# Optimization experiments

Measured on AMD Instinct MI355X. Metric: run time of the kernel, lower is better.

## Reference

```python
import jax, jax.numpy as jnp
import numpy as np

N_NODES = 100000
N_EDGES = 1600000
D_IN = 64
D_OUT = 64
EDGE_DIM = 1


def setup_inputs() -> dict:
    key = jax.random.key(0)
    ks = jax.random.split(key, 6)
    x = jax.random.normal(ks[0], (N_NODES, D_IN), dtype=jnp.float32)
    edge_index = jax.random.randint(ks[1], (2, N_EDGES), 0, N_NODES, dtype=jnp.int64)
    edge_attr = jax.random.uniform(ks[2], (N_EDGES, EDGE_DIM), dtype=jnp.float32)
    # xavier-uniform-ish weight
    limit = float(np.sqrt(6.0 / (D_IN + D_OUT)))
    weight = jax.random.uniform(ks[3], (D_IN, D_OUT), minval=-limit, maxval=limit, dtype=jnp.float32)
    lim2 = float(np.sqrt(1.0 / EDGE_DIM))
    ew_W = jax.random.uniform(ks[4], (EDGE_DIM, D_OUT), minval=-lim2, maxval=lim2, dtype=jnp.float32)
    ew_b = jnp.zeros((D_OUT,), dtype=jnp.float32)
    bias = jnp.zeros((D_OUT,), dtype=jnp.float32)
    return {"x": x, "edge_index": edge_index, "edge_attr": edge_attr,
            "weight": weight, "ew_W": ew_W, "ew_b": ew_b, "bias": bias}


def reference(x, edge_index, edge_attr, weight, ew_W, ew_b, bias):
    n_nodes = x.shape[0]
    src = edge_index[0]  # i: message source
    dst = edge_index[1]  # j: message destination
    x_t = x @ weight                                   # [N, D_OUT]
    edge_w = jax.nn.sigmoid(edge_attr @ ew_W + ew_b)   # [E, D_OUT]
    msg = x_t[src] * edge_w                            # [E, D_OUT] gather-multiply
    out = jax.ops.segment_sum(msg, dst, num_segments=n_nodes)  # scatter-add
    return out + bias
```

## Files before the change

kernel.cpp:

```cpp
#include <hip/hip_runtime.h>
#include <hip/hip_bf16.h>
#include <math.h>

#define D 64
#define SLOTS 32
#define SPILL_CAP 65536

typedef __hip_bfloat16 bf16;
typedef __attribute__((ext_vector_type(8))) short bf16x8;
typedef __attribute__((ext_vector_type(4))) float f32x4;

static __device__ __forceinline__ short f2bf(float f) {
    unsigned u = __float_as_uint(f);
    u = (u + 0x7FFFu + ((u >> 16) & 1u)) >> 16;
    return (short)u;
}
static __device__ __forceinline__ float bf2f(unsigned short h) {
    return __uint_as_float(((unsigned)h) << 16);
}
static __device__ __forceinline__ float fsig(float a, float nwd, float nbd) {
    float e = __expf(fmaf(a, nwd, nbd));
    return __builtin_amdgcn_rcpf(1.f + e);
}

__global__ __launch_bounds__(256) void gemm_hist_kernel(const float* __restrict__ x,
                                                        const float* __restrict__ W,
                                                        const int* __restrict__ ei,
                                                        const float* __restrict__ ea,
                                                        bf16* __restrict__ xt,
                                                        int* __restrict__ counts,
                                                        long long* __restrict__ rankv,
                                                        int n_nodes, int n_edges,
                                                        int hist_blocks) {
    __shared__ float Ws[64 * 64];

    if ((int)blockIdx.x < hist_blocks) {
        const int gid = blockIdx.x * blockDim.x + threadIdx.x;
        const int nth = hist_blocks * blockDim.x;
        for (int e = gid; e < n_edges; e += nth) {
            int dst = ei[n_edges + e];
            unsigned v = ((unsigned)min((int)(ea[e] * 32768.f), 32767) << 17) | (unsigned)ei[e];
            int r = atomicAdd(&counts[dst], 1);
            rankv[e] = ((long long)v << 32) | (unsigned)r;
        }
        return;
    }

    const int bid = blockIdx.x - hist_blocks;
    {
        const float4* src = reinterpret_cast<const float4*>(W);
        float4* dstp = reinterpret_cast<float4*>(Ws);
        for (int i = threadIdx.x; i < 1024; i += 256) dstp[i] = src[i];
    }
    __syncthreads();

    const int lane  = threadIdx.x & 63;
    const int wv    = threadIdx.x >> 6;
    const int m0    = bid * 64 + wv * 16;
    const int half  = lane >> 4;
    const int idx16 = lane & 15;
    const int k0    = half * 8;

    bf16x8 bfrag[4][2];
#pragma unroll
    for (int t = 0; t < 4; ++t) {
#pragma unroll
        for (int h = 0; h < 2; ++h) {
            bf16x8 f;
#pragma unroll
            for (int j = 0; j < 8; ++j)
                f[j] = f2bf(Ws[(h * 32 + k0 + j) * 64 + t * 16 + idx16]);
            bfrag[t][h] = f;
        }
    }

    const int am = m0 + idx16;
    const bool valid = (am < n_nodes);
    const float* arow = x + (size_t)(valid ? am : 0) * 64;

    f32x4 acc[4] = {{0.f, 0.f, 0.f, 0.f}, {0.f, 0.f, 0.f, 0.f},
                    {0.f, 0.f, 0.f, 0.f}, {0.f, 0.f, 0.f, 0.f}};

#pragma unroll
    for (int h = 0; h < 2; ++h) {
        bf16x8 afrag = {0, 0, 0, 0, 0, 0, 0, 0};
        if (valid) {
            float4 p0 = *reinterpret_cast<const float4*>(arow + h * 32 + k0);
            float4 p1 = *reinterpret_cast<const float4*>(arow + h * 32 + k0 + 4);
            afrag[0] = f2bf(p0.x); afrag[1] = f2bf(p0.y);
            afrag[2] = f2bf(p0.z); afrag[3] = f2bf(p0.w);
            afrag[4] = f2bf(p1.x); afrag[5] = f2bf(p1.y);
            afrag[6] = f2bf(p1.z); afrag[7] = f2bf(p1.w);
        }
#pragma unroll
        for (int t = 0; t < 4; ++t)
            acc[t] = __builtin_amdgcn_mfma_f32_16x16x32_bf16(afrag, bfrag[t][h],
                                                             acc[t], 0, 0, 0);
    }

    const int srow0 = m0 + half * 4;
#pragma unroll
    for (int r = 0; r < 4; ++r) {
        int row = srow0 + r;
        if (row < n_nodes) {
#pragma unroll
            for (int t = 0; t < 4; ++t)
                xt[(size_t)row * 64 + t * 16 + idx16] = __float2bfloat16(acc[t][r]);
        }
    }
}

__global__ __launch_bounds__(256) void fill_kernel(const int* __restrict__ ei,
                                                   const long long* __restrict__ rankv,
                                                   unsigned* __restrict__ csr,
                                                   long long* __restrict__ spill,
                                                   int* __restrict__ spillcnt,
                                                   int n_edges) {
    int e = blockIdx.x * blockDim.x + threadIdx.x;
    if (e >= n_edges) return;
    long long rv = rankv[e];
    int r = (int)(unsigned)rv;
    unsigned v = (unsigned)(rv >> 32);
    int dst = ei[n_edges + e];
    if (r < SLOTS) {
        __builtin_nontemporal_store(v, csr + (((unsigned)dst) << 5) + r);
    } else {
        int sp = atomicAdd(spillcnt, 1);
        if (sp < SPILL_CAP) spill[sp] = ((long long)v << 17) | (unsigned)dst;
    }
}

__global__ __launch_bounds__(256) void gather_kernel(const int* __restrict__ counts,
                                                     const unsigned* __restrict__ csr,
                                                     const bf16* __restrict__ xt,
                                                     const float* __restrict__ ewW,
                                                     const float* __restrict__ ewb,
                                                     const float* __restrict__ bias,
                                                     float* __restrict__ out,
                                                     int n_nodes) {
    const int lane  = threadIdx.x & 63;
    const int sub   = lane >> 4;
    const int l     = lane & 15;
    const int d0    = l * 4;
    const int wavei = (blockIdx.x * blockDim.x + threadIdx.x) >> 6;
    const int node  = wavei * 4 + sub;
    if (node >= n_nodes) return;

    const float4 wv4 = *reinterpret_cast<const float4*>(ewW + d0);
    const float4 bv4 = *reinterpret_cast<const float4*>(ewb + d0);
    const float nw0 = -wv4.x, nw1 = -wv4.y, nw2 = -wv4.z, nw3 = -wv4.w;
    const float nb0 = -bv4.x, nb1 = -bv4.y, nb2 = -bv4.z, nb3 = -bv4.w;
    const float s15 = 1.f / 32768.f;

    int deg = counts[node];
    if (deg > SLOTS) deg = SLOTS;
    const unsigned base = ((unsigned)node) << 5;

    float acc0 = 0.f, acc1 = 0.f, acc2 = 0.f, acc3 = 0.f;
    int k = 0;
    for (; k + 8 <= deg; k += 8) {
        unsigned q[8];
        ushort4 rv[8];
#pragma unroll
        for (int j = 0; j < 8; ++j)
            q[j] = __builtin_nontemporal_load(csr + base + k + j);
#pragma unroll
        for (int j = 0; j < 8; ++j) {
            unsigned off = ((q[j] & 0x1FFFFu) << 6) + d0;
            rv[j] = *reinterpret_cast<const ushort4*>(xt + off);
        }
#pragma unroll
        for (int j = 0; j < 8; ++j) {
            float a = (float)(q[j] >> 17) * s15;
            acc0 = fmaf(bf2f(rv[j].x), fsig(a, nw0, nb0), acc0);
            acc1 = fmaf(bf2f(rv[j].y), fsig(a, nw1, nb1), acc1);
            acc2 = fmaf(bf2f(rv[j].z), fsig(a, nw2, nb2), acc2);
            acc3 = fmaf(bf2f(rv[j].w), fsig(a, nw3, nb3), acc3);
        }
    }
    for (; k + 4 <= deg; k += 4) {
        unsigned q[4];
        ushort4 rv[4];
#pragma unroll
        for (int j = 0; j < 4; ++j)
            q[j] = __builtin_nontemporal_load(csr + base + k + j);
#pragma unroll
        for (int j = 0; j < 4; ++j) {
            unsigned off = ((q[j] & 0x1FFFFu) << 6) + d0;
            rv[j] = *reinterpret_cast<const ushort4*>(xt + off);
        }
#pragma unroll
        for (int j = 0; j < 4; ++j) {
            float a = (float)(q[j] >> 17) * s15;
            acc0 = fmaf(bf2f(rv[j].x), fsig(a, nw0, nb0), acc0);
            acc1 = fmaf(bf2f(rv[j].y), fsig(a, nw1, nb1), acc1);
            acc2 = fmaf(bf2f(rv[j].z), fsig(a, nw2, nb2), acc2);
            acc3 = fmaf(bf2f(rv[j].w), fsig(a, nw3, nb3), acc3);
        }
    }
    for (; k < deg; ++k) {
        unsigned q = __builtin_nontemporal_load(csr + base + k);
        unsigned off = ((q & 0x1FFFFu) << 6) + d0;
        ushort4 rv = *reinterpret_cast<const ushort4*>(xt + off);
        float a = (float)(q >> 17) * s15;
        acc0 = fmaf(bf2f(rv.x), fsig(a, nw0, nb0), acc0);
        acc1 = fmaf(bf2f(rv.y), fsig(a, nw1, nb1), acc1);
        acc2 = fmaf(bf2f(rv.z), fsig(a, nw2, nb2), acc2);
        acc3 = fmaf(bf2f(rv.w), fsig(a, nw3, nb3), acc3);
    }
    f32x4 o;
    o.x = acc0 + bias[d0 + 0];
    o.y = acc1 + bias[d0 + 1];
    o.z = acc2 + bias[d0 + 2];
    o.w = acc3 + bias[d0 + 3];
    __builtin_nontemporal_store(o, reinterpret_cast<f32x4*>(out + (size_t)node * 64 + d0));
}

__global__ __launch_bounds__(256) void spill_kernel(const long long* __restrict__ spill,
                                                    const int* __restrict__ spillcnt,
                                                    const bf16* __restrict__ xt,
                                                    const float* __restrict__ ewW,
                                                    const float* __restrict__ ewb,
                                                    float* __restrict__ out) {
    int n = *spillcnt;
    if (n > SPILL_CAP) n = SPILL_CAP;
    const int gid = blockIdx.x * blockDim.x + threadIdx.x;
    const int d0 = (gid & 15) * 4;
    const int estride = (gridDim.x * blockDim.x) >> 4;
    const float s15 = 1.f / 32768.f;
    for (int e = gid >> 4; e < n; e += estride) {
        long long s = spill[e];
        int dst = (int)(s & 0x1FFFF);
        unsigned v = (unsigned)(s >> 17);
        int src = (int)(v & 0x1FFFFu);
        float a = (float)(v >> 17) * s15;
        float* op = out + (size_t)dst * 64 + d0;
        const bf16* xp = xt + (size_t)src * 64 + d0;
#pragma unroll
        for (int j = 0; j < 4; ++j) {
            float w = fsig(a, -ewW[d0 + j], -ewb[d0 + j]);
            unsafeAtomicAdd(op + j, __bfloat162float(xp[j]) * w);
        }
    }
}

__global__ __launch_bounds__(256) void init_out_kernel(float* __restrict__ out,
                                                       const float* __restrict__ bias,
                                                       int n_f4) {
    int i = blockIdx.x * blockDim.x + threadIdx.x;
    if (i >= n_f4) return;
    float4 b4 = reinterpret_cast<const float4*>(bias)[i & 15];
    reinterpret_cast<float4*>(out)[i] = b4;
}

__global__ __launch_bounds__(256) void edge_atomic_kernel(const int* __restrict__ ei,
                                                          const float* __restrict__ ea,
                                                          const bf16* __restrict__ xt,
                                                          const float* __restrict__ ewW,
                                                          const float* __restrict__ ewb,
                                                          float* __restrict__ out,
                                                          int n_edges) {
    const int gid = blockIdx.x * blockDim.x + threadIdx.x;
    const int d0 = (gid & 15) * 4;
    int e = gid >> 4;
    const int estride = (gridDim.x * blockDim.x) >> 4;
    for (; e < n_edges; e += estride) {
        const int src = ei[e];
        const int dst = ei[n_edges + e];
        const float a = ea[e];
        float xv0 = __bfloat162float(xt[(size_t)src * 64 + d0 + 0]);
        float xv1 = __bfloat162float(xt[(size_t)src * 64 + d0 + 1]);
        float xv2 = __bfloat162float(xt[(size_t)src * 64 + d0 + 2]);
        float xv3 = __bfloat162float(xt[(size_t)src * 64 + d0 + 3]);
        float w0 = fsig(a, -ewW[d0 + 0], -ewb[d0 + 0]);
        float w1 = fsig(a, -ewW[d0 + 1], -ewb[d0 + 1]);
        float w2 = fsig(a, -ewW[d0 + 2], -ewb[d0 + 2]);
        float w3 = fsig(a, -ewW[d0 + 3], -ewb[d0 + 3]);
        float* op = out + (size_t)dst * 64 + d0;
        unsafeAtomicAdd(op + 0, xv0 * w0);
        unsafeAtomicAdd(op + 1, xv1 * w1);
        unsafeAtomicAdd(op + 2, xv2 * w2);
        unsafeAtomicAdd(op + 3, xv3 * w3);
    }
}

extern "C" void kernel_launch(void* const* d_in, const int* in_sizes, int n_in,
                              void* d_out, int out_size, void* d_ws, size_t ws_size,
                              hipStream_t stream) {
    const float* x      = (const float*)d_in[0];
    const int*   ei     = (const int*)d_in[1];
    const float* ea     = (const float*)d_in[2];
    const float* weight = (const float*)d_in[3];
    const float* ewW    = (const float*)d_in[4];
    const float* ewb    = (const float*)d_in[5];
    const float* bias   = (const float*)d_in[6];
    float* out = (float*)d_out;

    const int n_nodes = in_sizes[0] / D;
    const int n_edges = in_sizes[2];

    char* ws = (char*)d_ws;
    const size_t xt_bytes    = (size_t)n_nodes * D * sizeof(bf16);
    const size_t cnt_off     = (xt_bytes + 7) & ~(size_t)7;
    const size_t cnt_bytes   = ((size_t)n_nodes + 2) * sizeof(int);
    size_t csr_off           = (cnt_off + cnt_bytes + 7) & ~(size_t)7;
    const size_t csr_bytes   = (size_t)n_nodes * SLOTS * sizeof(unsigned);
    size_t rankv_off         = (csr_off + csr_bytes + 7) & ~(size_t)7;
    const size_t rankv_bytes = (size_t)n_edges * sizeof(long long);
    size_t spill_off         = (rankv_off + rankv_bytes + 7) & ~(size_t)7;
    const size_t spill_bytes = (size_t)SPILL_CAP * sizeof(long long);
    const size_t need        = spill_off + spill_bytes;

    bf16*      xt      = (bf16*)(ws);
    int*       counts  = (int*)(ws + cnt_off);
    int*       spillc  = counts + n_nodes;
    unsigned*  csr     = (unsigned*)(ws + csr_off);
    long long* rankv   = (long long*)(ws + rankv_off);
    long long* spill   = (long long*)(ws + spill_off);

    const bool have_ws = (ws_size >= need);
    const int gemm_blocks = (n_nodes + 63) / 64;
    const int hist_blocks = 512;

    if (have_ws) {
        (void)hipMemsetAsync(counts, 0, cnt_bytes, stream);
        gemm_hist_kernel<<<hist_blocks + gemm_blocks, 256, 0, stream>>>(
            x, weight, ei, ea, xt, counts, rankv, n_nodes, n_edges, hist_blocks);
        fill_kernel<<<(n_edges + 255) / 256, 256, 0, stream>>>(ei, rankv, csr,
                                                               spill, spillc, n_edges);
        const int n_waves = (n_nodes + 3) / 4;
        const int gth = n_waves * 64;
        gather_kernel<<<(gth + 255) / 256, 256, 0, stream>>>(counts, csr, xt, ewW, ewb,
                                                             bias, out, n_nodes);
        spill_kernel<<<64, 256, 0, stream>>>(spill, spillc, xt, ewW, ewb, out);
    } else {
        gemm_hist_kernel<<<gemm_blocks, 256, 0, stream>>>(
            x, weight, ei, ea, xt, nullptr, nullptr, n_nodes, 0, 0);
        int n_f4 = n_nodes * (D / 4);
        init_out_kernel<<<(n_f4 + 255) / 256, 256, 0, stream>>>(out, bias, n_f4);
        edge_atomic_kernel<<<4096, 256, 0, stream>>>(ei, ea, xt, ewW, ewb, out, n_edges);
    }
}
```

Measured before the change: 178.6 us.

## Pad per-node counters to cache lines and shrink rank buffer to bytes

Per-node atomic counters are now spaced 16 ints (64 bytes) apart so concurrent atomics from different nodes don't share a cache line. The histogram pass writes only an 8-bit rank per edge instead of a 64-bit packed value. The fill pass now reads edge_attr and the source index itself to build the CSR entry. This cuts intermediate write/read traffic but makes the counter memset 16x larger and adds extra input reads in fill.

```diff
diff --git a/kernel.cpp b/kernel.cpp
--- a/kernel.cpp
+++ b/kernel.cpp
@@ -5,6 +5,7 @@
 #define D 64
 #define SLOTS 32
 #define SPILL_CAP 65536
+#define CSTRIDE 16
 
 typedef __hip_bfloat16 bf16;
 typedef __attribute__((ext_vector_type(8))) short bf16x8;
@@ -26,10 +27,9 @@
 __global__ __launch_bounds__(256) void gemm_hist_kernel(const float* __restrict__ x,
                                                         const float* __restrict__ W,
                                                         const int* __restrict__ ei,
-                                                        const float* __restrict__ ea,
                                                         bf16* __restrict__ xt,
                                                         int* __restrict__ counts,
-                                                        long long* __restrict__ rankv,
+                                                        unsigned char* __restrict__ rank8,
                                                         int n_nodes, int n_edges,
                                                         int hist_blocks) {
     __shared__ float Ws[64 * 64];
@@ -39,9 +39,8 @@
         const int nth = hist_blocks * blockDim.x;
         for (int e = gid; e < n_edges; e += nth) {
             int dst = ei[n_edges + e];
-            unsigned v = ((unsigned)min((int)(ea[e] * 32768.f), 32767) << 17) | (unsigned)ei[e];
-            int r = atomicAdd(&counts[dst], 1);
-            rankv[e] = ((long long)v << 32) | (unsigned)r;
+            int r = atomicAdd(&counts[dst << 4], 1);
+            rank8[e] = (unsigned char)min(r, 255);
         }
         return;
     }
@@ -111,17 +110,17 @@
 }
 
 __global__ __launch_bounds__(256) void fill_kernel(const int* __restrict__ ei,
-                                                   const long long* __restrict__ rankv,
+                                                   const float* __restrict__ ea,
+                                                   const unsigned char* __restrict__ rank8,
                                                    unsigned* __restrict__ csr,
                                                    long long* __restrict__ spill,
                                                    int* __restrict__ spillcnt,
                                                    int n_edges) {
     int e = blockIdx.x * blockDim.x + threadIdx.x;
     if (e >= n_edges) return;
-    long long rv = rankv[e];
-    int r = (int)(unsigned)rv;
-    unsigned v = (unsigned)(rv >> 32);
+    int r = rank8[e];
     int dst = ei[n_edges + e];
+    unsigned v = ((unsigned)min((int)(ea[e] * 32768.f), 32767) << 17) | (unsigned)ei[e];
     if (r < SLOTS) {
         __builtin_nontemporal_store(v, csr + (((unsigned)dst) << 5) + r);
     } else {
@@ -152,7 +151,7 @@
     const float nb0 = -bv4.x, nb1 = -bv4.y, nb2 = -bv4.z, nb3 = -bv4.w;
     const float s15 = 1.f / 32768.f;
 
-    int deg = counts[node];
+    int deg = counts[node << 4];
     if (deg > SLOTS) deg = SLOTS;
     const unsigned base = ((unsigned)node) << 5;
 
@@ -301,22 +300,22 @@
 
     char* ws = (char*)d_ws;
     const size_t xt_bytes    = (size_t)n_nodes * D * sizeof(bf16);
-    const size_t cnt_off     = (xt_bytes + 7) & ~(size_t)7;
-    const size_t cnt_bytes   = ((size_t)n_nodes + 2) * sizeof(int);
-    size_t csr_off           = (cnt_off + cnt_bytes + 7) & ~(size_t)7;
+    const size_t cnt_off     = (xt_bytes + 63) & ~(size_t)63;
+    const size_t cnt_bytes   = ((size_t)n_nodes * CSTRIDE + 16) * sizeof(int);
+    size_t csr_off           = (cnt_off + cnt_bytes + 63) & ~(size_t)63;
     const size_t csr_bytes   = (size_t)n_nodes * SLOTS * sizeof(unsigned);
-    size_t rankv_off         = (csr_off + csr_bytes + 7) & ~(size_t)7;
-    const size_t rankv_bytes = (size_t)n_edges * sizeof(long long);
-    size_t spill_off         = (rankv_off + rankv_bytes + 7) & ~(size_t)7;
+    size_t rank_off          = (csr_off + csr_bytes + 63) & ~(size_t)63;
+    const size_t rank_bytes  = (size_t)n_edges;
+    size_t spill_off         = (rank_off + rank_bytes + 7) & ~(size_t)7;
     const size_t spill_bytes = (size_t)SPILL_CAP * sizeof(long long);
     const size_t need        = spill_off + spill_bytes;
 
-    bf16*      xt      = (bf16*)(ws);
-    int*       counts  = (int*)(ws + cnt_off);
-    int*       spillc  = counts + n_nodes;
-    unsigned*  csr     = (unsigned*)(ws + csr_off);
-    long long* rankv   = (long long*)(ws + rankv_off);
-    long long* spill   = (long long*)(ws + spill_off);
+    bf16*          xt     = (bf16*)(ws);
+    int*           counts = (int*)(ws + cnt_off);
+    int*           spillc = counts + (size_t)n_nodes * CSTRIDE;
+    unsigned*      csr    = (unsigned*)(ws + csr_off);
+    unsigned char* rank8  = (unsigned char*)(ws + rank_off);
+    long long*     spill  = (long long*)(ws + spill_off);
 
     const bool have_ws = (ws_size >= need);
     const int gemm_blocks = (n_nodes + 63) / 64;
@@ -325,8 +324,8 @@
     if (have_ws) {
         (void)hipMemsetAsync(counts, 0, cnt_bytes, stream);
         gemm_hist_kernel<<<hist_blocks + gemm_blocks, 256, 0, stream>>>(
-            x, weight, ei, ea, xt, counts, rankv, n_nodes, n_edges, hist_blocks);
-        fill_kernel<<<(n_edges + 255) / 256, 256, 0, stream>>>(ei, rankv, csr,
+            x, weight, ei, xt, counts, rank8, n_nodes, n_edges, hist_blocks);
+        fill_kernel<<<(n_edges + 255) / 256, 256, 0, stream>>>(ei, ea, rank8, csr,
                                                                spill, spillc, n_edges);
         const int n_waves = (n_nodes + 3) / 4;
         const int gth = n_waves * 64;
@@ -335,7 +334,7 @@
         spill_kernel<<<64, 256, 0, stream>>>(spill, spillc, xt, ewW, ewb, out);
     } else {
         gemm_hist_kernel<<<gemm_blocks, 256, 0, stream>>>(
-            x, weight, ei, ea, xt, nullptr, nullptr, n_nodes, 0, 0);
+            x, weight, ei, xt, nullptr, nullptr, n_nodes, 0, 0);
         int n_f4 = n_nodes * (D / 4);
         init_out_kernel<<<(n_f4 + 255) / 256, 256, 0, stream>>>(out, bias, n_f4);
         edge_atomic_kernel<<<4096, 256, 0, stream>>>(ei, ea, xt, ewW, ewb, out, n_edges);
```

Result: no change. 175.9 us (-1.5%).
